# Kernel optimization log

Hardware: AMD Instinct MI355X
Metric: run time of the kernel (lower is better)

Reference implementation:

```python
import jax, jax.numpy as jnp
import numpy as np

BN_EPS = 1e-05


def setup_inputs() -> dict:
    key = jax.random.key(0)
    ks = jax.random.split(key, 6)
    B, IN, OUT = 8192, 4096, 4096
    x = jax.random.normal(ks[0], (B, IN), dtype=jnp.float32)
    weight = jax.random.normal(ks[1], (OUT, IN), dtype=jnp.float32)
    bn_gamma = jax.random.uniform(ks[2], (OUT,), dtype=jnp.float32, minval=0.5, maxval=1.5)
    bn_beta = jax.random.normal(ks[3], (OUT,), dtype=jnp.float32)
    bn_mean = jax.random.normal(ks[4], (OUT,), dtype=jnp.float32)
    bn_var = jax.random.uniform(ks[5], (OUT,), dtype=jnp.float32, minval=0.1, maxval=2.0)
    return {"x": x, "weight": weight, "bn_gamma": bn_gamma, "bn_beta": bn_beta,
            "bn_mean": bn_mean, "bn_var": bn_var}


def reference(x, weight, bn_gamma, bn_beta, bn_mean, bn_var):
    # deterministic +/-1 binarization of activations and weights (eval path)
    x_bin = jnp.sign(x)
    w_bin = jnp.sign(weight)
    # binary linear: [B, IN] @ [IN, OUT] -> [B, OUT]
    out = jnp.einsum('bi,oi->bo', x_bin, w_bin)
    # exact (non-folded) BatchNorm using running stats
    std = jnp.sqrt(bn_var + BN_EPS)
    out = (out - bn_mean) / std * bn_gamma + bn_beta
    return out
```

## Files before the change

### kernel.cpp

```cpp
#include <hip/hip_runtime.h>
#include <stdint.h>
#include <stddef.h>


#define BN_EPS 1e-5f
typedef int   v4i __attribute__((ext_vector_type(4)));
typedef float v4f __attribute__((ext_vector_type(4)));
typedef unsigned int u32;

__global__ void bn_prep_kernel(const float* __restrict__ g, const float* __restrict__ b,
                               const float* __restrict__ m, const float* __restrict__ v,
                               float* __restrict__ scale, float* __restrict__ bias, int n) {
  int i = blockIdx.x * blockDim.x + threadIdx.x;
  if (i >= n) return;
  float s = g[i] * rsqrtf(v[i] + BN_EPS);
  scale[i] = s;
  bias[i] = b[i] - m[i] * s;
}

__global__ __launch_bounds__(256) void pack_sign_fp4_kernel(
    const uint4* __restrict__ in, uint4* __restrict__ outp, int n32) {
  int t = blockIdx.x * blockDim.x + threadIdx.x;
  if (t >= n32) return;
  const uint4* p = in + (size_t)t * 8;
  u32 w[4];
#pragma unroll
  for (int j = 0; j < 4; ++j) {
    uint4 u0 = p[2 * j];
    uint4 u1 = p[2 * j + 1];
    u32 h0 = 0x2222u | ((u0.x >> 28) & 0x8u) | (((u0.y >> 28) & 0x8u) << 4)
                     | (((u0.z >> 28) & 0x8u) << 8) | (((u0.w >> 28) & 0x8u) << 12);
    u32 h1 = 0x2222u | ((u1.x >> 28) & 0x8u) | (((u1.y >> 28) & 0x8u) << 4)
                     | (((u1.z >> 28) & 0x8u) << 8) | (((u1.w >> 28) & 0x8u) << 12);
    w[j] = h0 | (h1 << 16);
  }
  uint4 o; o.x = w[0]; o.y = w[1]; o.z = w[2]; o.w = w[3];
  outp[t] = o;
}


#define BAR() asm volatile("s_barrier" ::: "memory")
#define WAITV(n) asm volatile("s_waitcnt vmcnt(" #n ")" ::: "memory")
#define LGKM0() asm volatile("s_waitcnt lgkmcnt(0)" ::: "memory")

#define MFMA16x16(accv, av, bv) \
  asm("v_mfma_f32_16x16x128_f8f6f4 %0, %1, %2, %0 cbsz:4 blgp:4" \
      : "+v"(accv) : "v"(av), "v"(bv))

__global__ __launch_bounds__(1024, 4) void bgemm_fp4_w16(
    const int8_t* __restrict__ A4, const int8_t* __restrict__ B4,
    const float* __restrict__ scale, const float* __restrict__ bias,
    float* __restrict__ out, int M, int N, int RB ) {
  __shared__ __align__(16) int8_t lds[131072];

  const int tid = threadIdx.x;
  const int lane = tid & 63;
  const int wid = tid >> 6;
  const int wm = wid >> 2;
  const int wn = wid & 3;

  const int nbx = N >> 8;
  const int nwg = (M >> 8) * nbx;
  const int cpx = nwg >> 3;
  const int bid = (int)blockIdx.x;
  const int swz = (bid & 7) * cpx + (bid >> 3);
  const int row0 = (swz / nbx) << 8;
  const int col0 = (swz % nbx) << 8;

  const int ln15 = lane & 15;
  const int kcs = (((lane >> 4) ^ ((ln15 >> 1) & 3)) << 4);
  const int aoff = (wm * 64 + ln15) * 64 + kcs;
  const int boff = (wn * 64 + ln15) * 64 + kcs;

  const int srow = wid * 16 + (lane >> 2);
  const int sch = (((lane & 3) ^ ((lane >> 3) & 3)) << 4);
  const int ldw = wid << 10;

  const int8_t* aSt = A4 + (size_t)(row0 + srow) * RB + sch;
  const int8_t* bSt = B4 + (size_t)(col0 + srow) * RB + sch;

  v4f acc[4][4];
#pragma unroll
  for (int i = 0; i < 4; ++i)
#pragma unroll
    for (int n = 0; n < 4; ++n) { v4f z = {0.f, 0.f, 0.f, 0.f}; acc[i][n] = z; }

#define STAGE(s) do {                                                                 \
  const int bb_ = ((s) & 3) * 16384;                                                  \
  __builtin_amdgcn_global_load_lds(                                                   \
      (const __attribute__((address_space(1))) uint32_t*)(aSt + (size_t)(s) * 64),    \
      (__attribute__((address_space(3))) uint32_t*)(lds + bb_ + ldw), 16, 0, 0);      \
  __builtin_amdgcn_global_load_lds(                                                   \
      (const __attribute__((address_space(1))) uint32_t*)(bSt + (size_t)(s) * 64),    \
      (__attribute__((address_space(3))) uint32_t*)(lds + 65536 + bb_ + ldw), 16, 0, 0); \
} while (0)

#define COMPUTE(q) do {                                                               \
  const int8_t* ap_ = lds + (q) * 16384 + aoff;                                       \
  const int8_t* bp_ = lds + 65536 + (q) * 16384 + boff;                               \
  v4i Bv0 = *(const v4i*)(bp_);        v4i Bv1 = *(const v4i*)(bp_ + 1024);           \
  v4i Bv2 = *(const v4i*)(bp_ + 2048); v4i Bv3 = *(const v4i*)(bp_ + 3072);           \
  __builtin_amdgcn_s_setprio(1);                                                      \
  _Pragma("unroll")                                                                   \
  for (int m_ = 0; m_ < 4; ++m_) {                                                    \
    v4i Av = *(const v4i*)(ap_ + m_ * 1024);                                          \
    MFMA16x16(acc[m_][0], Av, Bv0);                                                   \
    MFMA16x16(acc[m_][1], Av, Bv1);                                                   \
    MFMA16x16(acc[m_][2], Av, Bv2);                                                   \
    MFMA16x16(acc[m_][3], Av, Bv3);                                                   \
  }                                                                                   \
  __builtin_amdgcn_s_setprio(0);                                                      \
} while (0)

  const int NT = RB >> 6;

  STAGE(0); STAGE(1); STAGE(2);
  WAITV(4);
  BAR();

  for (int t = 0; t < NT - 3; ++t) {
    STAGE(t + 3);
    COMPUTE(t & 3);
    LGKM0();
    WAITV(4);
    BAR();
  }
  COMPUTE((NT - 3) & 3); LGKM0(); WAITV(2); BAR();
  COMPUTE((NT - 2) & 3); LGKM0(); WAITV(0); BAR();
  COMPUTE((NT - 1) & 3);
  asm volatile("s_nop 7\n\ts_nop 7" :::);

  const int cw = col0 + wn * 64;
  float scv[4], biv[4];
#pragma unroll
  for (int n = 0; n < 4; ++n) {
    int c = cw + n * 16 + ln15;
    scv[n] = scale[c];
    biv[n] = bias[c];
  }
#pragma unroll
  for (int i = 0; i < 4; ++i) {
    const int r0 = row0 + wm * 64 + i * 16 + ((lane >> 4) << 2);
#pragma unroll
    for (int reg = 0; reg < 4; ++reg) {
      float* orow = out + (size_t)(r0 + reg) * N;
#pragma unroll
      for (int n = 0; n < 4; ++n)
        orow[cw + n * 16 + ln15] = fmaf(acc[i][n][reg], scv[n], biv[n]);
    }
  }

#undef STAGE
#undef COMPUTE
}

extern "C" void kernel_launch(void* const* d_in, const int* in_sizes, int n_in,
                              void* d_out, int out_size, void* d_ws, size_t ws_size,
                              hipStream_t stream) {
  const float* x = (const float*)d_in[0];
  const float* w = (const float*)d_in[1];
  const float* gamma = (const float*)d_in[2];
  const float* beta = (const float*)d_in[3];
  const float* mean = (const float*)d_in[4];
  const float* var = (const float*)d_in[5];
  float* out = (float*)d_out;

  const int OUT = in_sizes[2];
  const int IN = in_sizes[1] / OUT;
  const int B = in_sizes[0] / IN;
  const int RB = IN / 2;

  int8_t* a4 = (int8_t*)d_ws;
  int8_t* b4 = a4 + (size_t)B * RB;
  float* scale = (float*)(b4 + (size_t)OUT * RB);
  float* bias = scale + OUT;

  const int n32x = B * (IN / 32);
  const int n32w = OUT * (IN / 32);
  pack_sign_fp4_kernel<<<(n32x + 255) / 256, 256, 0, stream>>>(
      (const uint4*)x, (uint4*)a4, n32x);
  pack_sign_fp4_kernel<<<(n32w + 255) / 256, 256, 0, stream>>>(
      (const uint4*)w, (uint4*)b4, n32w);
  bn_prep_kernel<<<(OUT + 255) / 256, 256, 0, stream>>>(
      gamma, beta, mean, var, scale, bias, OUT);

  dim3 grid((B >> 8) * (OUT >> 8));
  bgemm_fp4_w16<<<grid, 1024, 0, stream>>>(a4, b4, scale, bias, out, B, OUT, RB);
}
```

Before: 124.8 us.

## Load B fragments directly from global in MFMA-ready tiled layout, bypassing LDS

The weight packing kernel now writes the fp4 weights in a tiled layout, 16 output columns per k-chunk, so each lane's MFMA B fragment sits in one contiguous 16-byte spot. The GEMM then loads B fragments straight into registers one iteration ahead instead of staging them through LDS. This halves LDS use, cutting LDS traffic and shared-memory footprint. In exchange, each of the four row-waves in a workgroup issues the same B global loads, relying on cache, and global latency is now exposed on the B path with only one iteration of prefetch.

```diff
diff --git a/kernel.cpp b/kernel.cpp
--- a/kernel.cpp
+++ b/kernel.cpp
@@ -38,6 +38,28 @@
   outp[t] = o;
 }
 
+__global__ __launch_bounds__(256) void pack_sign_fp4_wtile(
+    const uint4* __restrict__ in, uint4* __restrict__ outp, int n32, int GR) {
+  int t = blockIdx.x * blockDim.x + threadIdx.x;
+  if (t >= n32) return;
+  const uint4* p = in + (size_t)t * 8;
+  u32 w[4];
+#pragma unroll
+  for (int j = 0; j < 4; ++j) {
+    uint4 u0 = p[2 * j];
+    uint4 u1 = p[2 * j + 1];
+    u32 h0 = 0x2222u | ((u0.x >> 28) & 0x8u) | (((u0.y >> 28) & 0x8u) << 4)
+                     | (((u0.z >> 28) & 0x8u) << 8) | (((u0.w >> 28) & 0x8u) << 12);
+    u32 h1 = 0x2222u | ((u1.x >> 28) & 0x8u) | (((u1.y >> 28) & 0x8u) << 4)
+                     | (((u1.z >> 28) & 0x8u) << 8) | (((u1.w >> 28) & 0x8u) << 12);
+    w[j] = h0 | (h1 << 16);
+  }
+  uint4 o; o.x = w[0]; o.y = w[1]; o.z = w[2]; o.w = w[3];
+  const int c = t / GR;
+  const int g = t - c * GR;
+  outp[(size_t)(c >> 4) * (GR * 16) + g * 16 + (c & 15)] = o;
+}
+
 
 #define BAR() asm volatile("s_barrier" ::: "memory")
 #define WAITV(n) asm volatile("s_waitcnt vmcnt(" #n ")" ::: "memory")
@@ -47,11 +69,11 @@
   asm("v_mfma_f32_16x16x128_f8f6f4 %0, %1, %2, %0 cbsz:4 blgp:4" \
       : "+v"(accv) : "v"(av), "v"(bv))
 
-__global__ __launch_bounds__(1024, 4) void bgemm_fp4_w16(
+__global__ __launch_bounds__(1024, 4) void bgemm_fp4_fm(
     const int8_t* __restrict__ A4, const int8_t* __restrict__ B4,
     const float* __restrict__ scale, const float* __restrict__ bias,
     float* __restrict__ out, int M, int N, int RB ) {
-  __shared__ __align__(16) int8_t lds[131072];
+  __shared__ __align__(16) int8_t lds[65536];
 
   const int tid = threadIdx.x;
   const int lane = tid & 63;
@@ -70,36 +92,38 @@
   const int ln15 = lane & 15;
   const int kcs = (((lane >> 4) ^ ((ln15 >> 1) & 3)) << 4);
   const int aoff = (wm * 64 + ln15) * 64 + kcs;
-  const int boff = (wn * 64 + ln15) * 64 + kcs;
 
   const int srow = wid * 16 + (lane >> 2);
   const int sch = (((lane & 3) ^ ((lane >> 3) & 3)) << 4);
   const int ldw = wid << 10;
 
   const int8_t* aSt = A4 + (size_t)(row0 + srow) * RB + sch;
-  const int8_t* bSt = B4 + (size_t)(col0 + srow) * RB + sch;
+  const size_t TS = (size_t)RB * 16;
+  const int8_t* bGl = B4 + (size_t)((col0 >> 4) + wn * 4) * TS + lane * 16;
 
   v4f acc[4][4];
 #pragma unroll
   for (int i = 0; i < 4; ++i)
 #pragma unroll
     for (int n = 0; n < 4; ++n) { v4f z = {0.f, 0.f, 0.f, 0.f}; acc[i][n] = z; }
+
+  v4i Bv0, Bv1, Bv2, Bv3;
 
 #define STAGE(s) do {                                                                 \
   const int bb_ = ((s) & 3) * 16384;                                                  \
   __builtin_amdgcn_global_load_lds(                                                   \
       (const __attribute__((address_space(1))) uint32_t*)(aSt + (size_t)(s) * 64),    \
       (__attribute__((address_space(3))) uint32_t*)(lds + bb_ + ldw), 16, 0, 0);      \
-  __builtin_amdgcn_global_load_lds(                                                   \
-      (const __attribute__((address_space(1))) uint32_t*)(bSt + (size_t)(s) * 64),    \
-      (__attribute__((address_space(3))) uint32_t*)(lds + 65536 + bb_ + ldw), 16, 0, 0); \
+} while (0)
+
+#define PREF_B(s) do {                                                                \
+  const int8_t* p_ = bGl + (size_t)(s) * 1024;                                        \
+  Bv0 = *(const v4i*)(p_);          Bv1 = *(const v4i*)(p_ + TS);                     \
+  Bv2 = *(const v4i*)(p_ + 2 * TS); Bv3 = *(const v4i*)(p_ + 3 * TS);                 \
 } while (0)
 
 #define COMPUTE(q) do {                                                               \
   const int8_t* ap_ = lds + (q) * 16384 + aoff;                                       \
-  const int8_t* bp_ = lds + 65536 + (q) * 16384 + boff;                               \
-  v4i Bv0 = *(const v4i*)(bp_);        v4i Bv1 = *(const v4i*)(bp_ + 1024);           \
-  v4i Bv2 = *(const v4i*)(bp_ + 2048); v4i Bv3 = *(const v4i*)(bp_ + 3072);           \
   __builtin_amdgcn_s_setprio(1);                                                      \
   _Pragma("unroll")                                                                   \
   for (int m_ = 0; m_ < 4; ++m_) {                                                    \
@@ -115,18 +139,20 @@
   const int NT = RB >> 6;
 
   STAGE(0); STAGE(1); STAGE(2);
-  WAITV(4);
+  PREF_B(0);
+  WAITV(6);
   BAR();
 
   for (int t = 0; t < NT - 3; ++t) {
     STAGE(t + 3);
     COMPUTE(t & 3);
+    PREF_B(t + 1);
     LGKM0();
-    WAITV(4);
+    WAITV(6);
     BAR();
   }
-  COMPUTE((NT - 3) & 3); LGKM0(); WAITV(2); BAR();
-  COMPUTE((NT - 2) & 3); LGKM0(); WAITV(0); BAR();
+  COMPUTE((NT - 3) & 3); PREF_B(NT - 2); LGKM0(); WAITV(4); BAR();
+  COMPUTE((NT - 2) & 3); PREF_B(NT - 1); LGKM0(); WAITV(4); BAR();
   COMPUTE((NT - 1) & 3);
   asm volatile("s_nop 7\n\ts_nop 7" :::);
 
@@ -151,6 +177,7 @@
   }
 
 #undef STAGE
+#undef PREF_B
 #undef COMPUTE
 }
 
@@ -169,21 +196,22 @@
   const int IN = in_sizes[1] / OUT;
   const int B = in_sizes[0] / IN;
   const int RB = IN / 2;
+  const int GR = IN / 32;
 
   int8_t* a4 = (int8_t*)d_ws;
   int8_t* b4 = a4 + (size_t)B * RB;
   float* scale = (float*)(b4 + (size_t)OUT * RB);
   float* bias = scale + OUT;
 
-  const int n32x = B * (IN / 32);
-  const int n32w = OUT * (IN / 32);
+  const int n32x = B * GR;
+  const int n32w = OUT * GR;
   pack_sign_fp4_kernel<<<(n32x + 255) / 256, 256, 0, stream>>>(
       (const uint4*)x, (uint4*)a4, n32x);
-  pack_sign_fp4_kernel<<<(n32w + 255) / 256, 256, 0, stream>>>(
-      (const uint4*)w, (uint4*)b4, n32w);
+  pack_sign_fp4_wtile<<<(n32w + 255) / 256, 256, 0, stream>>>(
+      (const uint4*)w, (uint4*)b4, n32w, GR);
   bn_prep_kernel<<<(OUT + 255) / 256, 256, 0, stream>>>(
       gamma, beta, mean, var, scale, bias, OUT);
 
   dim3 grid((B >> 8) * (OUT >> 8));
-  bgemm_fp4_w16<<<grid, 1024, 0, stream>>>(a4, b4, scale, bias, out, B, OUT, RB);
-}
+  bgemm_fp4_fm<<<grid, 1024, 0, stream>>>(a4, b4, scale, bias, out, B, OUT, RB);
+}
```

Result: slower. 136.2 us (+9.1%).

## Shrink GEMM tile to 128x256 with 512 threads and 3-stage LDS ring

Applied to the files above, without the earlier changes.

Changes the workgroup tile from 256x256 with 16 waves to 128x256 with 8 waves. LDS drops from 128KB to 72KB using a 3-deep buffer ring instead of 4, and the main loop is unrolled by three with fixed buffer indices. The smaller per-block LDS footprint is meant to let two workgroups share a CU and to double the grid size. The cost is less reuse of A and B per tile and a shallower prefetch depth. The unrolled loop assumes the tile count is of the form 3k+2, which holds for IN=4096 (NT=32).

```diff
diff --git a/kernel.cpp b/kernel.cpp
--- a/kernel.cpp
+++ b/kernel.cpp
@@ -47,11 +47,11 @@
   asm("v_mfma_f32_16x16x128_f8f6f4 %0, %1, %2, %0 cbsz:4 blgp:4" \
       : "+v"(accv) : "v"(av), "v"(bv))
 
-__global__ __launch_bounds__(1024, 4) void bgemm_fp4_w16(
+__global__ __launch_bounds__(512, 4) void bgemm_fp4_2b(
     const int8_t* __restrict__ A4, const int8_t* __restrict__ B4,
     const float* __restrict__ scale, const float* __restrict__ bias,
     float* __restrict__ out, int M, int N, int RB ) {
-  __shared__ __align__(16) int8_t lds[131072];
+  __shared__ __align__(16) int8_t lds[73728];
 
   const int tid = threadIdx.x;
   const int lane = tid & 63;
@@ -60,11 +60,11 @@
   const int wn = wid & 3;
 
   const int nbx = N >> 8;
-  const int nwg = (M >> 8) * nbx;
+  const int nwg = (M >> 7) * nbx;
   const int cpx = nwg >> 3;
   const int bid = (int)blockIdx.x;
   const int swz = (bid & 7) * cpx + (bid >> 3);
-  const int row0 = (swz / nbx) << 8;
+  const int row0 = (swz / nbx) << 7;
   const int col0 = (swz % nbx) << 8;
 
   const int ln15 = lane & 15;
@@ -72,12 +72,14 @@
   const int aoff = (wm * 64 + ln15) * 64 + kcs;
   const int boff = (wn * 64 + ln15) * 64 + kcs;
 
-  const int srow = wid * 16 + (lane >> 2);
+  const int srow = lane >> 2;
   const int sch = (((lane & 3) ^ ((lane >> 3) & 3)) << 4);
-  const int ldw = wid << 10;
+  const int ldwA = wid << 10;
+  const int ldwB = wid << 11;
 
-  const int8_t* aSt = A4 + (size_t)(row0 + srow) * RB + sch;
-  const int8_t* bSt = B4 + (size_t)(col0 + srow) * RB + sch;
+  const size_t rstrB = (size_t)16 * RB;
+  const int8_t* aSt = A4 + (size_t)(row0 + wid * 16 + srow) * RB + sch;
+  const int8_t* bSt = B4 + (size_t)(col0 + wid * 32 + srow) * RB + sch;
 
   v4f acc[4][4];
 #pragma unroll
@@ -85,19 +87,21 @@
 #pragma unroll
     for (int n = 0; n < 4; ++n) { v4f z = {0.f, 0.f, 0.f, 0.f}; acc[i][n] = z; }
 
-#define STAGE(s) do {                                                                 \
-  const int bb_ = ((s) & 3) * 16384;                                                  \
+#define STAGE(s, qa) do {                                                             \
   __builtin_amdgcn_global_load_lds(                                                   \
       (const __attribute__((address_space(1))) uint32_t*)(aSt + (size_t)(s) * 64),    \
-      (__attribute__((address_space(3))) uint32_t*)(lds + bb_ + ldw), 16, 0, 0);      \
+      (__attribute__((address_space(3))) uint32_t*)(lds + (qa) * 8192 + ldwA), 16, 0, 0); \
   __builtin_amdgcn_global_load_lds(                                                   \
       (const __attribute__((address_space(1))) uint32_t*)(bSt + (size_t)(s) * 64),    \
-      (__attribute__((address_space(3))) uint32_t*)(lds + 65536 + bb_ + ldw), 16, 0, 0); \
+      (__attribute__((address_space(3))) uint32_t*)(lds + 24576 + (qa) * 16384 + ldwB), 16, 0, 0); \
+  __builtin_amdgcn_global_load_lds(                                                   \
+      (const __attribute__((address_space(1))) uint32_t*)(bSt + rstrB + (size_t)(s) * 64), \
+      (__attribute__((address_space(3))) uint32_t*)(lds + 24576 + (qa) * 16384 + 1024 + ldwB), 16, 0, 0); \
 } while (0)
 
 #define COMPUTE(q) do {                                                               \
-  const int8_t* ap_ = lds + (q) * 16384 + aoff;                                       \
-  const int8_t* bp_ = lds + 65536 + (q) * 16384 + boff;                               \
+  const int8_t* ap_ = lds + (q) * 8192 + aoff;                                        \
+  const int8_t* bp_ = lds + 24576 + (q) * 16384 + boff;                               \
   v4i Bv0 = *(const v4i*)(bp_);        v4i Bv1 = *(const v4i*)(bp_ + 1024);           \
   v4i Bv2 = *(const v4i*)(bp_ + 2048); v4i Bv3 = *(const v4i*)(bp_ + 3072);           \
   __builtin_amdgcn_s_setprio(1);                                                      \
@@ -112,22 +116,27 @@
   __builtin_amdgcn_s_setprio(0);                                                      \
 } while (0)
 
+#define BODY(t, qc, qs) do {                                                          \
+  STAGE((t) + 2, qs);                                                                 \
+  COMPUTE(qc);                                                                        \
+  LGKM0();                                                                            \
+  WAITV(3);                                                                           \
+  BAR();                                                                              \
+} while (0)
+
   const int NT = RB >> 6;
 
-  STAGE(0); STAGE(1); STAGE(2);
-  WAITV(4);
+  STAGE(0, 0); STAGE(1, 1);
+  WAITV(3);
   BAR();
 
-  for (int t = 0; t < NT - 3; ++t) {
-    STAGE(t + 3);
-    COMPUTE(t & 3);
-    LGKM0();
-    WAITV(4);
-    BAR();
+  for (int t = 0; t < NT - 2; t += 3) {
+    BODY(t + 0, 0, 2);
+    BODY(t + 1, 1, 0);
+    BODY(t + 2, 2, 1);
   }
-  COMPUTE((NT - 3) & 3); LGKM0(); WAITV(2); BAR();
-  COMPUTE((NT - 2) & 3); LGKM0(); WAITV(0); BAR();
-  COMPUTE((NT - 1) & 3);
+  COMPUTE(0); LGKM0(); WAITV(0); BAR();
+  COMPUTE(1);
   asm volatile("s_nop 7\n\ts_nop 7" :::);
 
   const int cw = col0 + wn * 64;
@@ -152,6 +161,7 @@
 
 #undef STAGE
 #undef COMPUTE
+#undef BODY
 }
 
 extern "C" void kernel_launch(void* const* d_in, const int* in_sizes, int n_in,
@@ -184,6 +194,6 @@
   bn_prep_kernel<<<(OUT + 255) / 256, 256, 0, stream>>>(
       gamma, beta, mean, var, scale, bias, OUT);
 
-  dim3 grid((B >> 8) * (OUT >> 8));
-  bgemm_fp4_w16<<<grid, 1024, 0, stream>>>(a4, b4, scale, bias, out, B, OUT, RB);
+  dim3 grid((B >> 7) * (OUT >> 8));
+  bgemm_fp4_2b<<<grid, 512, 0, stream>>>(a4, b4, scale, bias, out, B, OUT, RB);
 }
```

Result: slower. 130.6 us (+4.6%).
